# Kernel optimization log

Hardware: AMD Instinct MI355X
Metric: run time of the kernel (lower is better)

## Reference

```python
import jax, jax.numpy as jnp
import numpy as np

B, S, H, L = 16, 512, 768, 4096

def setup_inputs() -> dict:
    key = jax.random.key(0)
    k1, k2, k3 = jax.random.split(key, 3)
    inputs = jax.random.normal(k1, (B, S, H), dtype=jnp.float32)
    # realistic variable-length masks: each sequence has length in [S//2, S]
    lengths = jax.random.randint(k2, (B,), S // 2, S + 1)
    masks = jnp.arange(S)[None, :] < lengths[:, None]  # [B, S] bool
    # xavier_uniform for Linear(H, L, bias=False): weight shape [L, H]
    limit = float(np.sqrt(6.0 / (H + L)))
    W = jax.random.uniform(k3, (L, H), minval=-limit, maxval=limit, dtype=jnp.float32)
    return {"inputs": inputs, "masks": masks, "W": W}

def reference(inputs, masks, W):
    # scores: Linear(inputs) -> [B,S,L], transposed to [B,L,S]
    scores = jnp.einsum("bsh,lh->bls", inputs, W)
    scores = jnp.where(masks[:, None, :], scores, -jnp.inf)
    attn = jax.nn.softmax(scores, axis=-1)  # over seq dim
    # weighted sum pooling: [B,L,S] @ [B,S,H] -> [B,L,H]
    return jnp.einsum("bls,bsh->blh", attn, inputs)
```

## Files before the change

kernel.cpp:

```cpp
#include <hip/hip_runtime.h>
#include <hip/hip_bf16.h>

#define Bn 16
#define Sn 512
#define Hn 768
#define Ln 4096

typedef __attribute__((ext_vector_type(8))) short bf16x8;
typedef __attribute__((ext_vector_type(4))) float f32x4;

using bf16 = __hip_bfloat16;

constexpr int BL = 64;

constexpr int SM_BYTES  = 81920;
constexpr int PH2_BUF   = 36864;
constexpr int WS_OFF_IN = 32768;
constexpr int P_OFF     = 0;
constexpr int XT_OFF    = 65536;
constexpr int REDM_OFF  = 73728;
constexpr int REDS_OFF  = 74240;

typedef const __attribute__((address_space(1))) unsigned int* gas_ptr;
typedef __attribute__((address_space(3))) unsigned int* las_ptr;

__device__ __forceinline__ void gld_lds16(const void* g, void* l) {
  __builtin_amdgcn_global_load_lds((gas_ptr)g, (las_ptr)l, 16, 0, 0);
}

__device__ __forceinline__ unsigned short bfbits(float x) {
  __hip_bfloat16 h = __float2bfloat16(x);
  unsigned short u;
  __builtin_memcpy(&u, &h, 2);
  return u;
}

union Pack8 { bf16 h[8]; uint4 u; };

__device__ inline uint4 cvt8(float4 a, float4 b) {
  Pack8 p;
  p.h[0] = __float2bfloat16(a.x); p.h[1] = __float2bfloat16(a.y);
  p.h[2] = __float2bfloat16(a.z); p.h[3] = __float2bfloat16(a.w);
  p.h[4] = __float2bfloat16(b.x); p.h[5] = __float2bfloat16(b.y);
  p.h[6] = __float2bfloat16(b.z); p.h[7] = __float2bfloat16(b.w);
  return p.u;
}

__global__ __launch_bounds__(256) void convert_x_kernel(
    const float* __restrict__ X, bf16* __restrict__ Xbf, bf16* __restrict__ XT) {
  __shared__ bf16 t[64][72];
  const int tid = threadIdx.x;
  const int b  = blockIdx.z;
  const int s0 = blockIdx.y * 64;
  const int h0 = blockIdx.x * 64;
  const int r = tid >> 2;
  const int p = tid & 3;
  const float* src = X + ((size_t)b * Sn + s0 + r) * Hn + h0 + p * 16;
  float4 a0 = *(const float4*)(src + 0);
  float4 a1 = *(const float4*)(src + 4);
  float4 a2 = *(const float4*)(src + 8);
  float4 a3 = *(const float4*)(src + 12);
  uint4 u0 = cvt8(a0, a1);
  uint4 u1 = cvt8(a2, a3);
  bf16* xb = Xbf + ((size_t)b * Sn + s0 + r) * Hn + h0 + p * 16;
  *(uint4*)(xb)     = u0;
  *(uint4*)(xb + 8) = u1;
  *(uint4*)&t[r][p * 16]     = u0;
  *(uint4*)&t[r][p * 16 + 8] = u1;
  __syncthreads();
  Pack8 o0, o1;
#pragma unroll
  for (int i = 0; i < 8; ++i) {
    o0.h[i] = t[p * 16 + i][r];
    o1.h[i] = t[p * 16 + 8 + i][r];
  }
  bf16* xt = XT + ((size_t)b * Hn + h0 + r) * Sn + s0 + p * 16;
  *(uint4*)(xt)     = o0.u;
  *(uint4*)(xt + 8) = o1.u;
}

__global__ __launch_bounds__(256) void convert_w_kernel(
    const float* __restrict__ W, bf16* __restrict__ Wbf) {
  const size_t i = ((size_t)blockIdx.x * 256 + threadIdx.x) * 8;
  float4 a0 = *(const float4*)(W + i);
  float4 a1 = *(const float4*)(W + i + 4);
  *(uint4*)(Wbf + i) = cvt8(a0, a1);
}

__global__ __launch_bounds__(256, 2) void attn_main_kernel(
    const int* __restrict__ masks,
    const bf16* __restrict__ Xbf, const bf16* __restrict__ XTg,
    const bf16* __restrict__ Wbf, float* __restrict__ out) {
  __shared__ char sm[SM_BYTES];
  const int tid  = threadIdx.x;
  const int w    = tid >> 6;
  const int lane = tid & 63;
  const int col  = lane & 15;
  const int quad = lane >> 4;
  const int lg   = w >> 1;
  const int sg   = w & 1;
  const int vb = (blockIdx.x & 7) * 128 + (blockIdx.x >> 3);
  const int b  = vb >> 6;
  const int l0 = (vb & 63) * BL;

  float bias_r[16];
  {
    const int* mrow = masks + b * Sn + sg * 256 + col;
#pragma unroll
    for (int nt = 0; nt < 16; ++nt)
      bias_r[nt] = mrow[nt * 16] ? 0.0f : -1e30f;
  }

  const f32x4 zero = {0.f, 0.f, 0.f, 0.f};
  f32x4 acc[2][16];
#pragma unroll
  for (int a = 0; a < 2; ++a)
#pragma unroll
    for (int nt = 0; nt < 16; ++nt) acc[a][nt] = zero;

  const int rr2 = lane >> 2;
  const int cc2 = (lane & 3) * 8;

#define STAGE2(BUFOFF, K0)                                                         \
  {                                                                                \
    const bf16* gx = Xbf + ((size_t)b * Sn + w * 128 + rr2) * Hn + (K0) + cc2;     \
    char* dx = sm + (BUFOFF) + (w * 128) * 64;                                     \
    _Pragma("unroll")                                                              \
    for (int i = 0; i < 8; ++i) {                                                  \
      gld_lds16(gx, dx);                                                           \
      gx += 16 * Hn;                                                               \
      dx += 16 * 64;                                                               \
    }                                                                              \
    const bf16* gw = Wbf + ((size_t)(l0 + w * 16 + rr2)) * Hn + (K0) + cc2;        \
    gld_lds16(gw, sm + (BUFOFF) + WS_OFF_IN + (w * 16) * 64);                      \
  }

#define PH2_COMPUTE(BUFOFF)                                                        \
  {                                                                                \
    const char* xs = sm + (BUFOFF);                                                \
    const char* ws = sm + (BUFOFF) + WS_OFF_IN;                                    \
    bf16x8 a0 = *(const bf16x8*)&ws[(lg * 32 + col) * 64 + quad * 16];             \
    bf16x8 a1 = *(const bf16x8*)&ws[(lg * 32 + 16 + col) * 64 + quad * 16];        \
    _Pragma("unroll")                                                              \
    for (int nt = 0; nt < 16; ++nt) {                                              \
      bf16x8 bf_ = *(const bf16x8*)&xs[(sg * 256 + nt * 16 + col) * 64 + quad * 16]; \
      acc[0][nt] = __builtin_amdgcn_mfma_f32_16x16x32_bf16(a0, bf_, acc[0][nt], 0, 0, 0); \
      acc[1][nt] = __builtin_amdgcn_mfma_f32_16x16x32_bf16(a1, bf_, acc[1][nt], 0, 0, 0); \
    }                                                                              \
  }

  STAGE2(0, 0);
  asm volatile("s_waitcnt vmcnt(0)" ::: "memory");
  __builtin_amdgcn_s_barrier();
  for (int k0 = 0; k0 < Hn; k0 += 64) {
    STAGE2(PH2_BUF, k0 + 32);
    PH2_COMPUTE(0);
    asm volatile("s_waitcnt vmcnt(0)" ::: "memory");
    __builtin_amdgcn_s_barrier();
    if (k0 + 64 < Hn) STAGE2(0, k0 + 64);
    PH2_COMPUTE(PH2_BUF);
    asm volatile("s_waitcnt vmcnt(0)" ::: "memory");
    __builtin_amdgcn_s_barrier();
  }
#undef STAGE2
#undef PH2_COMPUTE

  float* redm = (float*)&sm[REDM_OFF];
  float* reds = (float*)&sm[REDS_OFF];
  float mx[2][4];
#pragma unroll
  for (int a = 0; a < 2; ++a)
#pragma unroll
    for (int r = 0; r < 4; ++r) mx[a][r] = -3e38f;
#pragma unroll
  for (int a = 0; a < 2; ++a)
#pragma unroll
    for (int nt = 0; nt < 16; ++nt)
#pragma unroll
      for (int r = 0; r < 4; ++r) {
        acc[a][nt][r] += bias_r[nt];
        mx[a][r] = fmaxf(mx[a][r], acc[a][nt][r]);
      }
#pragma unroll
  for (int a = 0; a < 2; ++a)
#pragma unroll
    for (int r = 0; r < 4; ++r) {
      mx[a][r] = fmaxf(mx[a][r], __shfl_xor(mx[a][r], 1, 64));
      mx[a][r] = fmaxf(mx[a][r], __shfl_xor(mx[a][r], 2, 64));
      mx[a][r] = fmaxf(mx[a][r], __shfl_xor(mx[a][r], 4, 64));
      mx[a][r] = fmaxf(mx[a][r], __shfl_xor(mx[a][r], 8, 64));
    }
  if (col == 0) {
#pragma unroll
    for (int a = 0; a < 2; ++a)
#pragma unroll
      for (int r = 0; r < 4; ++r)
        redm[sg * 64 + lg * 32 + a * 16 + quad * 4 + r] = mx[a][r];
  }
  __syncthreads();
  float gmax[2][4], sum[2][4];
#pragma unroll
  for (int a = 0; a < 2; ++a)
#pragma unroll
    for (int r = 0; r < 4; ++r) {
      const int row = lg * 32 + a * 16 + quad * 4 + r;
      gmax[a][r] = fmaxf(redm[row], redm[64 + row]);
      sum[a][r] = 0.f;
    }
#pragma unroll
  for (int a = 0; a < 2; ++a)
#pragma unroll
    for (int nt = 0; nt < 16; ++nt)
#pragma unroll
      for (int r = 0; r < 4; ++r) {
        const float e = __expf(acc[a][nt][r] - gmax[a][r]);
        acc[a][nt][r] = e;
        sum[a][r] += e;
      }
#pragma unroll
  for (int a = 0; a < 2; ++a)
#pragma unroll
    for (int r = 0; r < 4; ++r) {
      sum[a][r] += __shfl_xor(sum[a][r], 1, 64);
      sum[a][r] += __shfl_xor(sum[a][r], 2, 64);
      sum[a][r] += __shfl_xor(sum[a][r], 4, 64);
      sum[a][r] += __shfl_xor(sum[a][r], 8, 64);
    }
  if (col == 0) {
#pragma unroll
    for (int a = 0; a < 2; ++a)
#pragma unroll
      for (int r = 0; r < 4; ++r)
        reds[sg * 64 + lg * 32 + a * 16 + quad * 4 + r] = sum[a][r];
  }
  __syncthreads();
  float rs[2][4];
#pragma unroll
  for (int a = 0; a < 2; ++a)
#pragma unroll
    for (int r = 0; r < 4; ++r) {
      const int row = lg * 32 + a * 16 + quad * 4 + r;
      rs[a][r] = 1.0f / (reds[row] + reds[64 + row]);
    }

  const int pi = col & 1;
#pragma unroll
  for (int a = 0; a < 2; ++a)
#pragma unroll
    for (int t = 0; t < 8; ++t)
#pragma unroll
      for (int r = 0; r < 4; ++r) {
        const float own0 = acc[a][2 * t][r];
        const float own1 = acc[a][2 * t + 1][r];
        const float p0 = __shfl_xor(own0, 1, 64);
        const float p1 = __shfl_xor(own1, 1, 64);
        const float lo = pi ? p1 : own0;
        const float hi = pi ? own1 : p0;
        const unsigned pk = (unsigned)bfbits(lo) | ((unsigned)bfbits(hi) << 16);
        const int nt_w = 2 * t + pi;
        const int row = lg * 32 + a * 16 + quad * 4 + r;
        const int sp = sg * 256 + nt_w * 16 + (col & ~1);
        const int slot = (sp >> 3) ^ (row & 7);
        *(unsigned*)&sm[P_OFF + row * 1024 + slot * 16 + (sp & 7) * 2] = pk;
      }

  for (int n0 = 0; n0 < Hn / 128; ++n0) {
    f32x4 oacc[2][4];
#pragma unroll
    for (int a = 0; a < 2; ++a)
#pragma unroll
      for (int nt = 0; nt < 4; ++nt) oacc[a][nt] = zero;
    for (int s0 = 0; s0 < Sn; s0 += 64) {
      __syncthreads();
      {
        const int r0 = w * 32;
        const int rr = lane >> 3;
        const int cc = lane & 7;
        const bf16* g = XTg + ((size_t)b * Hn + n0 * 128 + r0 + rr) * Sn + s0 + (cc ^ rr) * 8;
#pragma unroll
        for (int i = 0; i < 4; ++i) {
          gld_lds16(g, &sm[XT_OFF + (r0 + i * 8) * 128]);
          g += 8 * Sn;
        }
      }
      __syncthreads();
#pragma unroll
      for (int ks = 0; ks < 2; ++ks) {
        const int chunk = (s0 + ks * 32 + quad * 8) >> 3;
        bf16x8 pa[2];
#pragma unroll
        for (int a = 0; a < 2; ++a) {
          const int row = lg * 32 + a * 16 + col;
          const int slot = chunk ^ (row & 7);
          pa[a] = *(const bf16x8*)&sm[P_OFF + row * 1024 + slot * 16];
        }
#pragma unroll
        for (int nt = 0; nt < 4; ++nt) {
          const int hl = (nt * 2 + sg) * 16 + col;
          const int xslot = (ks * 4 + quad) ^ (hl & 7);
          bf16x8 xb = *(const bf16x8*)&sm[XT_OFF + hl * 128 + xslot * 16];
          oacc[0][nt] = __builtin_amdgcn_mfma_f32_16x16x32_bf16(pa[0], xb, oacc[0][nt], 0, 0, 0);
          oacc[1][nt] = __builtin_amdgcn_mfma_f32_16x16x32_bf16(pa[1], xb, oacc[1][nt], 0, 0, 0);
        }
      }
    }
#pragma unroll
    for (int a = 0; a < 2; ++a)
#pragma unroll
      for (int nt = 0; nt < 4; ++nt) {
        const int h = n0 * 128 + (nt * 2 + sg) * 16 + col;
        const int lbase = l0 + lg * 32 + a * 16 + quad * 4;
#pragma unroll
        for (int r = 0; r < 4; ++r)
          out[((size_t)b * Ln + lbase + r) * Hn + h] = oacc[a][nt][r] * rs[a][r];
      }
  }
}

__global__ __launch_bounds__(256) void attn_fallback_kernel(
    const float* __restrict__ X, const int* __restrict__ masks,
    const float* __restrict__ W, float* __restrict__ out) {
  __shared__ float sc[4][Sn];
  const int wv = threadIdx.x >> 6, lane = threadIdx.x & 63;
  const int gw = blockIdx.x * 4 + wv;
  const int b = gw / Ln, l = gw % Ln;
  float wreg[12];
#pragma unroll
  for (int j = 0; j < 12; ++j) wreg[j] = W[(size_t)l * Hn + j * 64 + lane];
  for (int s = 0; s < Sn; ++s) {
    const float* xr = X + ((size_t)b * Sn + s) * Hn;
    float p = 0.f;
#pragma unroll
    for (int j = 0; j < 12; ++j) p += xr[j * 64 + lane] * wreg[j];
#pragma unroll
    for (int off = 32; off > 0; off >>= 1) p += __shfl_xor(p, off, 64);
    if (lane == 0) sc[wv][s] = p;
  }
  __syncthreads();
  float m = -3e38f;
#pragma unroll
  for (int i = 0; i < 8; ++i) {
    const int s = lane * 8 + i;
    const float v = sc[wv][s] + (masks[b * Sn + s] ? 0.f : -1e30f);
    sc[wv][s] = v;
    m = fmaxf(m, v);
  }
#pragma unroll
  for (int off = 32; off > 0; off >>= 1) m = fmaxf(m, __shfl_xor(m, off, 64));
  __syncthreads();
  float sum = 0.f;
#pragma unroll
  for (int i = 0; i < 8; ++i) {
    const int s = lane * 8 + i;
    const float e = __expf(sc[wv][s] - m);
    sc[wv][s] = e;
    sum += e;
  }
#pragma unroll
  for (int off = 32; off > 0; off >>= 1) sum += __shfl_xor(sum, off, 64);
  const float rs = 1.0f / sum;
  __syncthreads();
  float o[12];
#pragma unroll
  for (int j = 0; j < 12; ++j) o[j] = 0.f;
  for (int s = 0; s < Sn; ++s) {
    const float p = sc[wv][s];
    const float* xr = X + ((size_t)b * Sn + s) * Hn;
#pragma unroll
    for (int j = 0; j < 12; ++j) o[j] += p * xr[j * 64 + lane];
  }
#pragma unroll
  for (int j = 0; j < 12; ++j)
    out[((size_t)b * Ln + l) * Hn + j * 64 + lane] = o[j] * rs;
}

extern "C" void kernel_launch(void* const* d_in, const int* in_sizes, int n_in,
                              void* d_out, int out_size, void* d_ws, size_t ws_size,
                              hipStream_t stream) {
  const float* X     = (const float*)d_in[0];
  const int*   masks = (const int*)d_in[1];
  const float* W     = (const float*)d_in[2];
  float* out = (float*)d_out;

  const size_t need = ((size_t)2 * Bn * Sn * Hn + (size_t)Ln * Hn) * sizeof(bf16);
  if (ws_size >= need) {
    bf16* Xbf = (bf16*)d_ws;
    bf16* XT  = Xbf + (size_t)Bn * Sn * Hn;
    bf16* Wbf = XT  + (size_t)Bn * Sn * Hn;
    convert_x_kernel<<<dim3(Hn / 64, Sn / 64, Bn), 256, 0, stream>>>(X, Xbf, XT);
    convert_w_kernel<<<dim3((Ln * Hn) / 2048), 256, 0, stream>>>(W, Wbf);
    attn_main_kernel<<<dim3(Bn * (Ln / BL)), 256, 0, stream>>>(masks, Xbf, XT, Wbf, out);
  } else {
    attn_fallback_kernel<<<dim3(Bn * Ln / 4), 256, 0, stream>>>(X, masks, W, out);
  }
}
```

Baseline: 372.4 us.

## Double-buffer XT tiles, keep P in registers, retile score GEMM per wave

```diff
diff --git a/kernel.cpp b/kernel.cpp
--- a/kernel.cpp
+++ b/kernel.cpp
@@ -13,13 +13,12 @@
 
 constexpr int BL = 64;
 
-constexpr int SM_BYTES  = 81920;
+constexpr int SM_BYTES  = 75776;
 constexpr int PH2_BUF   = 36864;
 constexpr int WS_OFF_IN = 32768;
 constexpr int P_OFF     = 0;
-constexpr int XT_OFF    = 65536;
 constexpr int REDM_OFF  = 73728;
-constexpr int REDS_OFF  = 74240;
+constexpr int REDS_OFF  = 74752;
 
 typedef const __attribute__((address_space(1))) unsigned int* gas_ptr;
 typedef __attribute__((address_space(3))) unsigned int* las_ptr;
@@ -103,20 +102,20 @@
   const int b  = vb >> 6;
   const int l0 = (vb & 63) * BL;
 
-  float bias_r[16];
+  float bias_r[8];
   {
-    const int* mrow = masks + b * Sn + sg * 256 + col;
-#pragma unroll
-    for (int nt = 0; nt < 16; ++nt)
+    const int* mrow = masks + b * Sn + w * 128 + col;
+#pragma unroll
+    for (int nt = 0; nt < 8; ++nt)
       bias_r[nt] = mrow[nt * 16] ? 0.0f : -1e30f;
   }
 
   const f32x4 zero = {0.f, 0.f, 0.f, 0.f};
-  f32x4 acc[2][16];
-#pragma unroll
-  for (int a = 0; a < 2; ++a)
-#pragma unroll
-    for (int nt = 0; nt < 16; ++nt) acc[a][nt] = zero;
+  f32x4 acc[4][8];
+#pragma unroll
+  for (int am = 0; am < 4; ++am)
+#pragma unroll
+    for (int nt = 0; nt < 8; ++nt) acc[am][nt] = zero;
 
   const int rr2 = lane >> 2;
   const int cc2 = (lane & 3) * 8;
@@ -139,14 +138,18 @@
   {                                                                                \
     const char* xs = sm + (BUFOFF);                                                \
     const char* ws = sm + (BUFOFF) + WS_OFF_IN;                                    \
-    bf16x8 a0 = *(const bf16x8*)&ws[(lg * 32 + col) * 64 + quad * 16];             \
-    bf16x8 a1 = *(const bf16x8*)&ws[(lg * 32 + 16 + col) * 64 + quad * 16];        \
+    bf16x8 aF[4], bF[8];                                                           \
     _Pragma("unroll")                                                              \
-    for (int nt = 0; nt < 16; ++nt) {                                              \
-      bf16x8 bf_ = *(const bf16x8*)&xs[(sg * 256 + nt * 16 + col) * 64 + quad * 16]; \
-      acc[0][nt] = __builtin_amdgcn_mfma_f32_16x16x32_bf16(a0, bf_, acc[0][nt], 0, 0, 0); \
-      acc[1][nt] = __builtin_amdgcn_mfma_f32_16x16x32_bf16(a1, bf_, acc[1][nt], 0, 0, 0); \
-    }                                                                              \
+    for (int am = 0; am < 4; ++am)                                                 \
+      aF[am] = *(const bf16x8*)&ws[(am * 16 + col) * 64 + quad * 16];              \
+    _Pragma("unroll")                                                              \
+    for (int nt = 0; nt < 8; ++nt)                                                 \
+      bF[nt] = *(const bf16x8*)&xs[(w * 128 + nt * 16 + col) * 64 + quad * 16];    \
+    _Pragma("unroll")                                                              \
+    for (int nt = 0; nt < 8; ++nt)                                                 \
+      _Pragma("unroll")                                                            \
+      for (int am = 0; am < 4; ++am)                                               \
+        acc[am][nt] = __builtin_amdgcn_mfma_f32_16x16x32_bf16(aF[am], bF[nt], acc[am][nt], 0, 0, 0); \
   }
 
   STAGE2(0, 0);
@@ -167,142 +170,161 @@
 
   float* redm = (float*)&sm[REDM_OFF];
   float* reds = (float*)&sm[REDS_OFF];
-  float mx[2][4];
-#pragma unroll
-  for (int a = 0; a < 2; ++a)
-#pragma unroll
-    for (int r = 0; r < 4; ++r) mx[a][r] = -3e38f;
-#pragma unroll
-  for (int a = 0; a < 2; ++a)
-#pragma unroll
-    for (int nt = 0; nt < 16; ++nt)
+  float mx[4][4];
+#pragma unroll
+  for (int am = 0; am < 4; ++am)
+#pragma unroll
+    for (int r = 0; r < 4; ++r) mx[am][r] = -3e38f;
+#pragma unroll
+  for (int am = 0; am < 4; ++am)
+#pragma unroll
+    for (int nt = 0; nt < 8; ++nt)
 #pragma unroll
       for (int r = 0; r < 4; ++r) {
-        acc[a][nt][r] += bias_r[nt];
-        mx[a][r] = fmaxf(mx[a][r], acc[a][nt][r]);
+        acc[am][nt][r] += bias_r[nt];
+        mx[am][r] = fmaxf(mx[am][r], acc[am][nt][r]);
       }
 #pragma unroll
-  for (int a = 0; a < 2; ++a)
+  for (int am = 0; am < 4; ++am)
 #pragma unroll
     for (int r = 0; r < 4; ++r) {
-      mx[a][r] = fmaxf(mx[a][r], __shfl_xor(mx[a][r], 1, 64));
-      mx[a][r] = fmaxf(mx[a][r], __shfl_xor(mx[a][r], 2, 64));
-      mx[a][r] = fmaxf(mx[a][r], __shfl_xor(mx[a][r], 4, 64));
-      mx[a][r] = fmaxf(mx[a][r], __shfl_xor(mx[a][r], 8, 64));
+      mx[am][r] = fmaxf(mx[am][r], __shfl_xor(mx[am][r], 1, 64));
+      mx[am][r] = fmaxf(mx[am][r], __shfl_xor(mx[am][r], 2, 64));
+      mx[am][r] = fmaxf(mx[am][r], __shfl_xor(mx[am][r], 4, 64));
+      mx[am][r] = fmaxf(mx[am][r], __shfl_xor(mx[am][r], 8, 64));
     }
   if (col == 0) {
 #pragma unroll
-    for (int a = 0; a < 2; ++a)
+    for (int am = 0; am < 4; ++am)
 #pragma unroll
       for (int r = 0; r < 4; ++r)
-        redm[sg * 64 + lg * 32 + a * 16 + quad * 4 + r] = mx[a][r];
-  }
-  __syncthreads();
-  float gmax[2][4], sum[2][4];
-#pragma unroll
-  for (int a = 0; a < 2; ++a)
+        redm[w * 64 + am * 16 + quad * 4 + r] = mx[am][r];
+  }
+  __syncthreads();
+  float gmax[4][4], sum[4][4];
+#pragma unroll
+  for (int am = 0; am < 4; ++am)
 #pragma unroll
     for (int r = 0; r < 4; ++r) {
-      const int row = lg * 32 + a * 16 + quad * 4 + r;
-      gmax[a][r] = fmaxf(redm[row], redm[64 + row]);
-      sum[a][r] = 0.f;
-    }
-#pragma unroll
-  for (int a = 0; a < 2; ++a)
-#pragma unroll
-    for (int nt = 0; nt < 16; ++nt)
+      const int row = am * 16 + quad * 4 + r;
+      gmax[am][r] = fmaxf(fmaxf(redm[row], redm[64 + row]),
+                          fmaxf(redm[128 + row], redm[192 + row]));
+      sum[am][r] = 0.f;
+    }
+#pragma unroll
+  for (int am = 0; am < 4; ++am)
+#pragma unroll
+    for (int nt = 0; nt < 8; ++nt)
 #pragma unroll
       for (int r = 0; r < 4; ++r) {
-        const float e = __expf(acc[a][nt][r] - gmax[a][r]);
-        acc[a][nt][r] = e;
-        sum[a][r] += e;
+        const float e = __expf(acc[am][nt][r] - gmax[am][r]);
+        acc[am][nt][r] = e;
+        sum[am][r] += e;
       }
 #pragma unroll
-  for (int a = 0; a < 2; ++a)
+  for (int am = 0; am < 4; ++am)
 #pragma unroll
     for (int r = 0; r < 4; ++r) {
-      sum[a][r] += __shfl_xor(sum[a][r], 1, 64);
-      sum[a][r] += __shfl_xor(sum[a][r], 2, 64);
-      sum[a][r] += __shfl_xor(sum[a][r], 4, 64);
-      sum[a][r] += __shfl_xor(sum[a][r], 8, 64);
+      sum[am][r] += __shfl_xor(sum[am][r], 1, 64);
+      sum[am][r] += __shfl_xor(sum[am][r], 2, 64);
+      sum[am][r] += __shfl_xor(sum[am][r], 4, 64);
+      sum[am][r] += __shfl_xor(sum[am][r], 8, 64);
     }
   if (col == 0) {
 #pragma unroll
-    for (int a = 0; a < 2; ++a)
+    for (int am = 0; am < 4; ++am)
 #pragma unroll
       for (int r = 0; r < 4; ++r)
-        reds[sg * 64 + lg * 32 + a * 16 + quad * 4 + r] = sum[a][r];
-  }
-  __syncthreads();
-  float rs[2][4];
-#pragma unroll
-  for (int a = 0; a < 2; ++a)
+        reds[w * 64 + am * 16 + quad * 4 + r] = sum[am][r];
+  }
+  __syncthreads();
+  float rs[4][4];
+#pragma unroll
+  for (int am = 0; am < 4; ++am)
 #pragma unroll
     for (int r = 0; r < 4; ++r) {
-      const int row = lg * 32 + a * 16 + quad * 4 + r;
-      rs[a][r] = 1.0f / (reds[row] + reds[64 + row]);
+      const int row = am * 16 + quad * 4 + r;
+      rs[am][r] = 1.0f / (reds[row] + reds[64 + row] + reds[128 + row] + reds[192 + row]);
     }
 
   const int pi = col & 1;
 #pragma unroll
-  for (int a = 0; a < 2; ++a)
-#pragma unroll
-    for (int t = 0; t < 8; ++t)
+  for (int am = 0; am < 4; ++am)
+#pragma unroll
+    for (int t = 0; t < 4; ++t)
 #pragma unroll
       for (int r = 0; r < 4; ++r) {
-        const float own0 = acc[a][2 * t][r];
-        const float own1 = acc[a][2 * t + 1][r];
+        const float own0 = acc[am][2 * t][r];
+        const float own1 = acc[am][2 * t + 1][r];
         const float p0 = __shfl_xor(own0, 1, 64);
         const float p1 = __shfl_xor(own1, 1, 64);
         const float lo = pi ? p1 : own0;
         const float hi = pi ? own1 : p0;
         const unsigned pk = (unsigned)bfbits(lo) | ((unsigned)bfbits(hi) << 16);
         const int nt_w = 2 * t + pi;
-        const int row = lg * 32 + a * 16 + quad * 4 + r;
-        const int sp = sg * 256 + nt_w * 16 + (col & ~1);
+        const int row = am * 16 + quad * 4 + r;
+        const int sp = w * 128 + nt_w * 16 + (col & ~1);
         const int slot = (sp >> 3) ^ (row & 7);
         *(unsigned*)&sm[P_OFF + row * 1024 + slot * 16 + (sp & 7) * 2] = pk;
       }
 
+  __syncthreads();
+
+  bf16x8 preg[2][16];
+#pragma unroll
+  for (int a = 0; a < 2; ++a) {
+    const int row = lg * 32 + a * 16 + col;
+#pragma unroll
+    for (int kf = 0; kf < 16; ++kf) {
+      const int slot = (kf * 4 + quad) ^ (row & 7);
+      preg[a][kf] = *(const bf16x8*)&sm[P_OFF + row * 1024 + slot * 16];
+    }
+  }
+  __syncthreads();
+
+  const int rr5 = lane >> 3;
+  const int cc5 = lane & 7;
+  auto stage_xt = [&](int bufoff, int n0, int s0) {
+    const int r0 = w * 32;
+    const bf16* g = XTg + ((size_t)b * Hn + n0 * 128 + r0 + rr5) * Sn + s0 + (cc5 ^ rr5) * 8;
+#pragma unroll
+    for (int i = 0; i < 4; ++i) {
+      gld_lds16(g, &sm[bufoff + (r0 + i * 8) * 128]);
+      g += 8 * Sn;
+    }
+  };
+
+  stage_xt(0, 0, 0);
+  asm volatile("s_waitcnt vmcnt(0)" ::: "memory");
+  __builtin_amdgcn_s_barrier();
+
   for (int n0 = 0; n0 < Hn / 128; ++n0) {
     f32x4 oacc[2][4];
 #pragma unroll
     for (int a = 0; a < 2; ++a)
 #pragma unroll
       for (int nt = 0; nt < 4; ++nt) oacc[a][nt] = zero;
-    for (int s0 = 0; s0 < Sn; s0 += 64) {
-      __syncthreads();
-      {
-        const int r0 = w * 32;
-        const int rr = lane >> 3;
-        const int cc = lane & 7;
-        const bf16* g = XTg + ((size_t)b * Hn + n0 * 128 + r0 + rr) * Sn + s0 + (cc ^ rr) * 8;
-#pragma unroll
-        for (int i = 0; i < 4; ++i) {
-          gld_lds16(g, &sm[XT_OFF + (r0 + i * 8) * 128]);
-          g += 8 * Sn;
-        }
-      }
-      __syncthreads();
+#pragma unroll
+    for (int s0i = 0; s0i < 8; ++s0i) {
+      const int par = s0i & 1;
+      if (s0i < 7)           stage_xt((par ^ 1) * 16384, n0, (s0i + 1) * 64);
+      else if (n0 < Hn / 128 - 1) stage_xt((par ^ 1) * 16384, n0 + 1, 0);
 #pragma unroll
       for (int ks = 0; ks < 2; ++ks) {
-        const int chunk = (s0 + ks * 32 + quad * 8) >> 3;
-        bf16x8 pa[2];
-#pragma unroll
-        for (int a = 0; a < 2; ++a) {
-          const int row = lg * 32 + a * 16 + col;
-          const int slot = chunk ^ (row & 7);
-          pa[a] = *(const bf16x8*)&sm[P_OFF + row * 1024 + slot * 16];
-        }
+        const int kf = s0i * 2 + ks;
+        const bf16x8 pa0 = preg[0][kf];
+        const bf16x8 pa1 = preg[1][kf];
 #pragma unroll
         for (int nt = 0; nt < 4; ++nt) {
           const int hl = (nt * 2 + sg) * 16 + col;
           const int xslot = (ks * 4 + quad) ^ (hl & 7);
-          bf16x8 xb = *(const bf16x8*)&sm[XT_OFF + hl * 128 + xslot * 16];
-          oacc[0][nt] = __builtin_amdgcn_mfma_f32_16x16x32_bf16(pa[0], xb, oacc[0][nt], 0, 0, 0);
-          oacc[1][nt] = __builtin_amdgcn_mfma_f32_16x16x32_bf16(pa[1], xb, oacc[1][nt], 0, 0, 0);
+          bf16x8 xb = *(const bf16x8*)&sm[par * 16384 + hl * 128 + xslot * 16];
+          oacc[0][nt] = __builtin_amdgcn_mfma_f32_16x16x32_bf16(pa0, xb, oacc[0][nt], 0, 0, 0);
+          oacc[1][nt] = __builtin_amdgcn_mfma_f32_16x16x32_bf16(pa1, xb, oacc[1][nt], 0, 0, 0);
         }
       }
+      asm volatile("s_waitcnt vmcnt(0)" ::: "memory");
+      __builtin_amdgcn_s_barrier();
     }
 #pragma unroll
     for (int a = 0; a < 2; ++a)
@@ -312,7 +334,7 @@
         const int lbase = l0 + lg * 32 + a * 16 + quad * 4;
 #pragma unroll
         for (int r = 0; r < 4; ++r)
-          out[((size_t)b * Ln + lbase + r) * Hn + h] = oacc[a][nt][r] * rs[a][r];
+          out[((size_t)b * Ln + lbase + r) * Hn + h] = oacc[a][nt][r] * rs[lg * 2 + a][r];
       }
   }
 }
```

After: 359.3 us. 3.5% less time.
